# Optimization experiments

Hardware: AMD Instinct MI355X
Metric: run time of the kernel (lower is better)

## Reference

```python
import jax, jax.numpy as jnp
import numpy as np

NUM_NODES = 100000
IN_DIM = 64
OUT_DIM = 64
NUM_EDGES = 1250000


def setup_inputs() -> dict:
    key = jax.random.key(0)
    k1, k2, k3, k4, k5 = jax.random.split(key, 5)
    x = jax.random.normal(k1, (NUM_NODES, IN_DIM), dtype=jnp.float32)
    edge_index = jax.random.randint(k2, (2, NUM_EDGES), 0, NUM_NODES, dtype=jnp.int32)
    # Linear params (PyTorch default init: uniform(-1/sqrt(in), 1/sqrt(in)))
    bound = 1.0 / np.sqrt(IN_DIM)
    W_self = jax.random.uniform(k3, (OUT_DIM, IN_DIM), minval=-bound, maxval=bound, dtype=jnp.float32)
    b_self = jax.random.uniform(k4, (OUT_DIM,), minval=-bound, maxval=bound, dtype=jnp.float32)
    W_neigh = jax.random.uniform(k5, (OUT_DIM, IN_DIM), minval=-bound, maxval=bound, dtype=jnp.float32)
    return {"x": x, "edge_index": edge_index, "W_self": W_self, "b_self": b_self, "W_neigh": W_neigh}


def reference(x, edge_index, W_self, b_self, W_neigh):
    # x: [N, D_in], edge_index: [2, E]
    src, dst = edge_index[0], edge_index[1]
    num_nodes = x.shape[0]
    x_src = x[src]  # [E, D_in] gather
    neigh_agg = jax.ops.segment_sum(x_src, dst, num_segments=num_nodes)  # [N, D_in]
    deg = jax.ops.segment_sum(jnp.ones_like(dst, dtype=x.dtype), dst, num_segments=num_nodes)
    deg = jnp.clip(deg, 1.0, None)[:, None]
    neigh_mean = neigh_agg / deg
    out = x @ W_self.T + b_self + neigh_mean @ W_neigh.T
    return jax.nn.relu(out)
```

## Files before the change

### kernel.cpp

```cpp
#include <hip/hip_runtime.h>


#define BKSH 9
#define BKN 512
#define NBMAX 256
#define CAPE 7168
#define WPT (CAPE / BKN)
#define CHUNK 8192
#define EPT (CHUNK / 256)

typedef __attribute__((ext_vector_type(8))) short short8;
typedef __attribute__((ext_vector_type(4))) float floatx4;

static __device__ inline unsigned short f2bf(float f) {
  union { float f; unsigned int u; } v;
  v.f = f;
  unsigned int r = v.u + 0x7FFFu + ((v.u >> 16) & 1u);
  return (unsigned short)(r >> 16);
}

static __device__ inline short8 pack8(float4 a, float4 b) {
  short8 s;
  s[0] = (short)f2bf(a.x); s[1] = (short)f2bf(a.y);
  s[2] = (short)f2bf(a.z); s[3] = (short)f2bf(a.w);
  s[4] = (short)f2bf(b.x); s[5] = (short)f2bf(b.y);
  s[6] = (short)f2bf(b.z); s[7] = (short)f2bf(b.w);
  return s;
}

static __device__ inline void add8(float* a, short8 sv) {
  union { short8 s; unsigned int u[4]; } c; c.s = sv;
#pragma unroll
  for (int i = 0; i < 4; ++i) {
    a[2 * i]     += __uint_as_float(c.u[i] << 16);
    a[2 * i + 1] += __uint_as_float(c.u[i] & 0xFFFF0000u);
  }
}

__global__ __launch_bounds__(256) void k1_prep(
    const float* __restrict__ x, unsigned short* __restrict__ xb, long long n,
    const float* __restrict__ Wself, const float* __restrict__ Wneigh,
    unsigned short* __restrict__ wsb, unsigned short* __restrict__ wnb,
    const int* __restrict__ src, const int* __restrict__ dst,
    int* __restrict__ cursor, int* __restrict__ ebuf, int E, int NB, int SCB) {
  __shared__ int h[NBMAX], loff[NBMAX], gbase[NBMAX];
  __shared__ int sbuf[CHUNK];
  int t = threadIdx.x;
  int bid = blockIdx.x;

  if (bid >= SCB) {
    long long i = ((long long)(bid - SCB) * 256 + t) * 8;
    if (i < n) {
      float4 a = *(const float4*)&x[i];
      float4 b = *(const float4*)&x[i + 4];
      *(short8*)&xb[i] = pack8(a, b);
    }
    if (bid == gridDim.x - 1) {
      for (int g = t; g < 512; g += 256) {
        const float* p = &Wself[g * 8];
        *(short8*)&wsb[g * 8] = pack8(*(const float4*)p, *(const float4*)(p + 4));
        const float* q = &Wneigh[g * 8];
        *(short8*)&wnb[g * 8] = pack8(*(const float4*)q, *(const float4*)(q + 4));
      }
    }
    return;
  }

  if (t < NBMAX) h[t] = 0;
  __syncthreads();

  int base = bid * CHUNK;
  int myd[EPT], mys[EPT];
#pragma unroll
  for (int i = 0; i < EPT; ++i) {
    int e = base + t + 256 * i;
    if (e < E) {
      myd[i] = dst[e];
      mys[i] = src[e];
      atomicAdd(&h[myd[i] >> BKSH], 1);
    } else myd[i] = -1;
  }
  __syncthreads();

  if (t < 64) {
    int i0 = 4 * t;
    int v0 = h[i0], v1 = h[i0 + 1], v2 = h[i0 + 2], v3 = h[i0 + 3];
    int s4 = v0 + v1 + v2 + v3, inc = s4;
#pragma unroll
    for (int off = 1; off < 64; off <<= 1) {
      int u = __shfl_up(inc, off, 64);
      if (t >= off) inc += u;
    }
    int ex = inc - s4;
    loff[i0] = ex; loff[i0 + 1] = ex + v0;
    loff[i0 + 2] = ex + v0 + v1; loff[i0 + 3] = ex + v0 + v1 + v2;
  }
  __syncthreads();

  if (t < NB) {
    if (h[t] > 0) gbase[t] = t * CAPE + atomicAdd(&cursor[t], h[t]);
  }
  if (t < NBMAX) h[t] = 0;
  __syncthreads();

#pragma unroll
  for (int i = 0; i < EPT; ++i) {
    if (myd[i] >= 0) {
      int b = myd[i] >> BKSH;
      int p = atomicAdd(&h[b], 1);
      sbuf[loff[b] + p] = mys[i] | ((myd[i] & (BKN - 1)) << 17);
    }
  }
  __syncthreads();

  int w = t >> 6, lane = t & 63;
  for (int b = w; b < NB; b += 4) {
    int c = h[b], lo = loff[b], go = gbase[b];
    for (int j = lane; j < c; j += 64)
      ebuf[go + j] = sbuf[lo + j];
  }
}

__global__ __launch_bounds__(512) void sb_csr(const int* __restrict__ cursor,
                                              const int* __restrict__ ebuf,
                                              int* __restrict__ col,
                                              int2* __restrict__ rowse, int N) {
  __shared__ int sbuf[CAPE];
  __shared__ int cnt[BKN];
  __shared__ int wsum[8];
  int b = blockIdx.x, t = threadIdx.x;
  int s = b * CAPE;
  int n = cursor[b];
  int e = s + n;

  int my[WPT];
#pragma unroll
  for (int i = 0; i < WPT; ++i) {
    int j = s + t + i * BKN;
    my[i] = (j < e) ? ebuf[j] : -1;
  }

  cnt[t] = 0;
  __syncthreads();
#pragma unroll
  for (int i = 0; i < WPT; ++i)
    if (my[i] >= 0) atomicAdd(&cnt[(my[i] >> 17) & (BKN - 1)], 1);
  __syncthreads();

  int v = cnt[t];
  int lane = t & 63, w = t >> 6;
  int inc = v;
#pragma unroll
  for (int o = 1; o < 64; o <<= 1) {
    int u = __shfl_up(inc, o, 64);
    if (lane >= o) inc += u;
  }
  if (lane == 63) wsum[w] = inc;
  __syncthreads();
  if (t < 8) {
    int s0 = wsum[t], incw = s0;
#pragma unroll
    for (int o = 1; o < 8; o <<= 1) {
      int u = __shfl_up(incw, o, 64);
      if (t >= o) incw += u;
    }
    wsum[t] = incw - s0;
  }
  __syncthreads();
  int ex = wsum[w] + inc - v;
  int node = (b << BKSH) + t;
  if (node < N) rowse[node] = make_int2(s + ex, v);
  __syncthreads();
  cnt[t] = ex;
  __syncthreads();

#pragma unroll
  for (int i = 0; i < WPT; ++i) {
    if (my[i] >= 0) {
      int nl = (my[i] >> 17) & (BKN - 1);
      int p = atomicAdd(&cnt[nl], 1);
      sbuf[p] = my[i] & 0x1FFFF;
    }
  }
  __syncthreads();

  for (int j = t; j < n; j += BKN) col[s + j] = sbuf[j];
}

__global__ __launch_bounds__(256) void gcn_gather(const unsigned short* __restrict__ xb,
                                                  const int2* __restrict__ rowse,
                                                  const int* __restrict__ col,
                                                  unsigned short* __restrict__ aggb,
                                                  int N) {
  int gid = blockIdx.x * 256 + threadIdx.x;
  int node = gid >> 6;
  if (node >= N) return;
  int lane = threadIdx.x & 63;
  int o = lane >> 3, d = lane & 7;
  int2 se = rowse[node];
  int s = se.x, c = se.y, e = s + c;

  float a[8] = {0.f, 0.f, 0.f, 0.f, 0.f, 0.f, 0.f, 0.f};
  float b2[8] = {0.f, 0.f, 0.f, 0.f, 0.f, 0.f, 0.f, 0.f};
  for (int j = s + o; j < e; j += 16) {
    int c0 = col[j];
    bool h2 = (j + 8) < e;
    int c1 = h2 ? col[j + 8] : c0;
    short8 v0 = *(const short8*)&xb[(long long)c0 * 64 + d * 8];
    short8 v1 = *(const short8*)&xb[(long long)c1 * 64 + d * 8];
    add8(a, v0);
    if (h2) add8(b2, v1);
  }
#pragma unroll
  for (int k = 0; k < 8; ++k) a[k] += b2[k];

#pragma unroll
  for (int m = 8; m <= 32; m <<= 1) {
#pragma unroll
    for (int k = 0; k < 8; ++k) a[k] += __shfl_xor(a[k], m, 64);
  }

  if (o == 0) {
    float inv = 1.0f / fmaxf((float)c, 1.0f);
    short8 r;
#pragma unroll
    for (int k = 0; k < 8; ++k) r[k] = (short)f2bf(a[k] * inv);
    *(short8*)&aggb[(long long)node * 64 + d * 8] = r;
  }
}

__global__ __launch_bounds__(256) void gcn_gemm(const unsigned short* __restrict__ xb,
                                                const unsigned short* __restrict__ aggb,
                                                const unsigned short* __restrict__ wsb,
                                                const float* __restrict__ bself,
                                                const unsigned short* __restrict__ wnb,
                                                float* __restrict__ out, int N) {
  int lane = threadIdx.x & 63;
  int w = threadIdx.x >> 6;
  int tb = blockIdx.x * 64 + w * 16;
  int m = lane & 15, q = lane >> 4;

  long long rowA = (long long)min(tb + m, N - 1) * 64;
  short8 ax[2], aa[2];
#pragma unroll
  for (int ks = 0; ks < 2; ++ks) {
    ax[ks] = *(const short8*)&xb[rowA + ks * 32 + q * 8];
    aa[ks] = *(const short8*)&aggb[rowA + ks * 32 + q * 8];
  }

#pragma unroll
  for (int nt = 0; nt < 4; ++nt) {
    int ob = nt * 16;
    long long rowB = (long long)(ob + m) * 64;
    floatx4 acc = {0.f, 0.f, 0.f, 0.f};
#pragma unroll
    for (int ks = 0; ks < 2; ++ks) {
      short8 bw = *(const short8*)&wsb[rowB + ks * 32 + q * 8];
      acc = __builtin_amdgcn_mfma_f32_16x16x32_bf16(ax[ks], bw, acc, 0, 0, 0);
      short8 bn = *(const short8*)&wnb[rowB + ks * 32 + q * 8];
      acc = __builtin_amdgcn_mfma_f32_16x16x32_bf16(aa[ks], bn, acc, 0, 0, 0);
    }
    float bias = bself[ob + m];
#pragma unroll
    for (int r = 0; r < 4; ++r) {
      int node = tb + q * 4 + r;
      if (node < N) {
        float v = acc[r] + bias;
        out[(long long)node * 64 + ob + m] = fmaxf(v, 0.f);
      }
    }
  }
}

extern "C" void kernel_launch(void* const* d_in, const int* in_sizes, int n_in,
                              void* d_out, int out_size, void* d_ws, size_t ws_size,
                              hipStream_t stream) {
  const float* x      = (const float*)d_in[0];
  const int*   eidx   = (const int*)d_in[1];
  const float* Wself  = (const float*)d_in[2];
  const float* bself  = (const float*)d_in[3];
  const float* Wneigh = (const float*)d_in[4];
  float* out = (float*)d_out;

  const int N = in_sizes[0] / 64;
  const int E = in_sizes[1] / 2;
  const int* src = eidx;
  const int* dst = eidx + E;
  const int NB = (N + BKN - 1) / BKN;

  unsigned short* xb   = (unsigned short*)d_ws;
  unsigned short* aggb = xb + (size_t)N * 64;
  int* cursor   = (int*)(aggb + (size_t)N * 64);
  unsigned short* wsb = (unsigned short*)(cursor + NBMAX);
  unsigned short* wnb = wsb + 4096;
  int2* rowse   = (int2*)(wnb + 4096);
  int* ebuf     = (int*)(rowse + N);
  int* col      = ebuf + (size_t)NB * CAPE;

  hipMemsetAsync(cursor, 0, NBMAX * sizeof(int), stream);

  long long nx = (long long)N * 64;
  const int SCB = (E + CHUNK - 1) / CHUNK;
  int xbl = (int)((nx / 8 + 255) / 256);
  k1_prep<<<SCB + xbl + 1, 256, 0, stream>>>(x, xb, nx, Wself, Wneigh, wsb, wnb,
                                             src, dst, cursor, ebuf, E, NB, SCB);
  sb_csr<<<NB, BKN, 0, stream>>>(cursor, ebuf, col, rowse, N);
  gcn_gather<<<(int)((nx + 255) / 256), 256, 0, stream>>>(xb, rowse, col, aggb, N);
  gcn_gemm<<<(N + 63) / 64, 256, 0, stream>>>(xb, aggb, wsb, bself, wnb, out, N);
}
```

Before: 168.9 us.

## Transform features before aggregation and fuse gather with final epilogue

Uses linearity of the mean aggregation: each node's x is multiplied by W_neigh (and W_self plus bias) up front, inside the first kernel's extra blocks. The edge gather then sums the transformed bf16 rows, and the same kernel adds the fp32 self term and applies ReLU. This removes the separate GEMM launch and the aggregate write and read. In exchange it writes a full fp32 self-term buffer and reads it back in the gather. The scatter chunk size is also halved, giving more scatter blocks.

Result: faster. 163.0 us (-3.5%).

```diff
diff --git a/kernel.cpp b/kernel.cpp
--- a/kernel.cpp
+++ b/kernel.cpp
@@ -6,7 +6,7 @@
 #define NBMAX 256
 #define CAPE 7168
 #define WPT (CAPE / BKN)
-#define CHUNK 8192
+#define CHUNK 4096
 #define EPT (CHUNK / 256)
 
 typedef __attribute__((ext_vector_type(8))) short short8;
@@ -37,30 +37,56 @@
   }
 }
 
-__global__ __launch_bounds__(256) void k1_prep(
-    const float* __restrict__ x, unsigned short* __restrict__ xb, long long n,
-    const float* __restrict__ Wself, const float* __restrict__ Wneigh,
-    unsigned short* __restrict__ wsb, unsigned short* __restrict__ wnb,
+__global__ __launch_bounds__(256) void k1_main(
+    const float* __restrict__ x,
+    const float* __restrict__ Wself, const float* __restrict__ bself,
+    const float* __restrict__ Wneigh,
+    float* __restrict__ yb, unsigned short* __restrict__ zb,
     const int* __restrict__ src, const int* __restrict__ dst,
-    int* __restrict__ cursor, int* __restrict__ ebuf, int E, int NB, int SCB) {
+    int* __restrict__ cursor, int* __restrict__ ebuf,
+    int E, int N, int NB, int SCB) {
   __shared__ int h[NBMAX], loff[NBMAX], gbase[NBMAX];
   __shared__ int sbuf[CHUNK];
   int t = threadIdx.x;
   int bid = blockIdx.x;
 
   if (bid >= SCB) {
-    long long i = ((long long)(bid - SCB) * 256 + t) * 8;
-    if (i < n) {
-      float4 a = *(const float4*)&x[i];
-      float4 b = *(const float4*)&x[i + 4];
-      *(short8*)&xb[i] = pack8(a, b);
-    }
-    if (bid == gridDim.x - 1) {
-      for (int g = t; g < 512; g += 256) {
-        const float* p = &Wself[g * 8];
-        *(short8*)&wsb[g * 8] = pack8(*(const float4*)p, *(const float4*)(p + 4));
-        const float* q = &Wneigh[g * 8];
-        *(short8*)&wnb[g * 8] = pack8(*(const float4*)q, *(const float4*)(q + 4));
+    int lane = t & 63;
+    int w = t >> 6;
+    int tb = (bid - SCB) * 64 + w * 16;
+    int m = lane & 15, q = lane >> 4;
+
+    long long rowA = (long long)min(tb + m, N - 1) * 64;
+    short8 ax[2];
+#pragma unroll
+    for (int ks = 0; ks < 2; ++ks) {
+      const float* xr = &x[rowA + ks * 32 + q * 8];
+      ax[ks] = pack8(*(const float4*)xr, *(const float4*)(xr + 4));
+    }
+
+#pragma unroll
+    for (int nt = 0; nt < 4; ++nt) {
+      int ob = nt * 16;
+      long long rowB = (long long)(ob + m) * 64;
+      floatx4 accs = {0.f, 0.f, 0.f, 0.f};
+      floatx4 accn = {0.f, 0.f, 0.f, 0.f};
+#pragma unroll
+      for (int ks = 0; ks < 2; ++ks) {
+        const float* pw = &Wself[rowB + ks * 32 + q * 8];
+        short8 bs = pack8(*(const float4*)pw, *(const float4*)(pw + 4));
+        accs = __builtin_amdgcn_mfma_f32_16x16x32_bf16(ax[ks], bs, accs, 0, 0, 0);
+        const float* pn = &Wneigh[rowB + ks * 32 + q * 8];
+        short8 bn = pack8(*(const float4*)pn, *(const float4*)(pn + 4));
+        accn = __builtin_amdgcn_mfma_f32_16x16x32_bf16(ax[ks], bn, accn, 0, 0, 0);
+      }
+      float bias = bself[ob + m];
+#pragma unroll
+      for (int r = 0; r < 4; ++r) {
+        int node = tb + q * 4 + r;
+        if (node < N) {
+          yb[(long long)node * 64 + ob + m] = accs[r] + bias;
+          zb[(long long)node * 64 + ob + m] = f2bf(accn[r]);
+        }
       }
     }
     return;
@@ -187,11 +213,12 @@
   for (int j = t; j < n; j += BKN) col[s + j] = sbuf[j];
 }
 
-__global__ __launch_bounds__(256) void gcn_gather(const unsigned short* __restrict__ xb,
-                                                  const int2* __restrict__ rowse,
-                                                  const int* __restrict__ col,
-                                                  unsigned short* __restrict__ aggb,
-                                                  int N) {
+__global__ __launch_bounds__(256) void gather_final(
+    const unsigned short* __restrict__ zb,
+    const int2* __restrict__ rowse,
+    const int* __restrict__ col,
+    const float* __restrict__ yb,
+    float* __restrict__ out, int N) {
   int gid = blockIdx.x * 256 + threadIdx.x;
   int node = gid >> 6;
   if (node >= N) return;
@@ -206,8 +233,8 @@
     int c0 = col[j];
     bool h2 = (j + 8) < e;
     int c1 = h2 ? col[j + 8] : c0;
-    short8 v0 = *(const short8*)&xb[(long long)c0 * 64 + d * 8];
-    short8 v1 = *(const short8*)&xb[(long long)c1 * 64 + d * 8];
+    short8 v0 = *(const short8*)&zb[(long long)c0 * 64 + d * 8];
+    short8 v1 = *(const short8*)&zb[(long long)c1 * 64 + d * 8];
     add8(a, v0);
     if (h2) add8(b2, v1);
   }
@@ -222,53 +249,20 @@
 
   if (o == 0) {
     float inv = 1.0f / fmaxf((float)c, 1.0f);
-    short8 r;
-#pragma unroll
-    for (int k = 0; k < 8; ++k) r[k] = (short)f2bf(a[k] * inv);
-    *(short8*)&aggb[(long long)node * 64 + d * 8] = r;
-  }
-}
-
-__global__ __launch_bounds__(256) void gcn_gemm(const unsigned short* __restrict__ xb,
-                                                const unsigned short* __restrict__ aggb,
-                                                const unsigned short* __restrict__ wsb,
-                                                const float* __restrict__ bself,
-                                                const unsigned short* __restrict__ wnb,
-                                                float* __restrict__ out, int N) {
-  int lane = threadIdx.x & 63;
-  int w = threadIdx.x >> 6;
-  int tb = blockIdx.x * 64 + w * 16;
-  int m = lane & 15, q = lane >> 4;
-
-  long long rowA = (long long)min(tb + m, N - 1) * 64;
-  short8 ax[2], aa[2];
-#pragma unroll
-  for (int ks = 0; ks < 2; ++ks) {
-    ax[ks] = *(const short8*)&xb[rowA + ks * 32 + q * 8];
-    aa[ks] = *(const short8*)&aggb[rowA + ks * 32 + q * 8];
-  }
-
-#pragma unroll
-  for (int nt = 0; nt < 4; ++nt) {
-    int ob = nt * 16;
-    long long rowB = (long long)(ob + m) * 64;
-    floatx4 acc = {0.f, 0.f, 0.f, 0.f};
-#pragma unroll
-    for (int ks = 0; ks < 2; ++ks) {
-      short8 bw = *(const short8*)&wsb[rowB + ks * 32 + q * 8];
-      acc = __builtin_amdgcn_mfma_f32_16x16x32_bf16(ax[ks], bw, acc, 0, 0, 0);
-      short8 bn = *(const short8*)&wnb[rowB + ks * 32 + q * 8];
-      acc = __builtin_amdgcn_mfma_f32_16x16x32_bf16(aa[ks], bn, acc, 0, 0, 0);
-    }
-    float bias = bself[ob + m];
-#pragma unroll
-    for (int r = 0; r < 4; ++r) {
-      int node = tb + q * 4 + r;
-      if (node < N) {
-        float v = acc[r] + bias;
-        out[(long long)node * 64 + ob + m] = fmaxf(v, 0.f);
-      }
-    }
+    long long ro = (long long)node * 64 + d * 8;
+    float4 y0 = *(const float4*)&yb[ro];
+    float4 y1 = *(const float4*)&yb[ro + 4];
+    float4 r0, r1;
+    r0.x = fmaxf(y0.x + a[0] * inv, 0.f);
+    r0.y = fmaxf(y0.y + a[1] * inv, 0.f);
+    r0.z = fmaxf(y0.z + a[2] * inv, 0.f);
+    r0.w = fmaxf(y0.w + a[3] * inv, 0.f);
+    r1.x = fmaxf(y1.x + a[4] * inv, 0.f);
+    r1.y = fmaxf(y1.y + a[5] * inv, 0.f);
+    r1.z = fmaxf(y1.z + a[6] * inv, 0.f);
+    r1.w = fmaxf(y1.w + a[7] * inv, 0.f);
+    *(float4*)&out[ro] = r0;
+    *(float4*)&out[ro + 4] = r1;
   }
 }
 
@@ -288,23 +282,20 @@
   const int* dst = eidx + E;
   const int NB = (N + BKN - 1) / BKN;
 
-  unsigned short* xb   = (unsigned short*)d_ws;
-  unsigned short* aggb = xb + (size_t)N * 64;
-  int* cursor   = (int*)(aggb + (size_t)N * 64);
-  unsigned short* wsb = (unsigned short*)(cursor + NBMAX);
-  unsigned short* wnb = wsb + 4096;
-  int2* rowse   = (int2*)(wnb + 4096);
-  int* ebuf     = (int*)(rowse + N);
-  int* col      = ebuf + (size_t)NB * CAPE;
+  float* yb = (float*)d_ws;
+  unsigned short* zb = (unsigned short*)(yb + (size_t)N * 64);
+  int* cursor = (int*)(zb + (size_t)N * 64);
+  int2* rowse = (int2*)(cursor + NBMAX);
+  int* ebuf   = (int*)(rowse + N);
+  int* col    = ebuf + (size_t)NB * CAPE;
 
   hipMemsetAsync(cursor, 0, NBMAX * sizeof(int), stream);
 
-  long long nx = (long long)N * 64;
   const int SCB = (E + CHUNK - 1) / CHUNK;
-  int xbl = (int)((nx / 8 + 255) / 256);
-  k1_prep<<<SCB + xbl + 1, 256, 0, stream>>>(x, xb, nx, Wself, Wneigh, wsb, wnb,
-                                             src, dst, cursor, ebuf, E, NB, SCB);
+  const int GB = (N + 63) / 64;
+  k1_main<<<SCB + GB, 256, 0, stream>>>(x, Wself, bself, Wneigh, yb, zb,
+                                        src, dst, cursor, ebuf, E, N, NB, SCB);
   sb_csr<<<NB, BKN, 0, stream>>>(cursor, ebuf, col, rowse, N);
-  gcn_gather<<<(int)((nx + 255) / 256), 256, 0, stream>>>(xb, rowse, col, aggb, N);
-  gcn_gemm<<<(N + 63) / 64, 256, 0, stream>>>(xb, aggb, wsb, bself, wnb, out, N);
-}
+  gather_final<<<(int)(((long long)N * 64 + 255) / 256), 256, 0, stream>>>(
+      zb, rowse, col, yb, out, N);
+}
```
